# Kernel optimization log

Hardware: AMD Instinct MI355X
Metric: run time of the kernel (lower is better)

Reference implementation:

```python
import jax, jax.numpy as jnp
import numpy as np
from jax.scipy.linalg import expm

HIDDEN = 1024
STATE = 64
INTER = 4096
EPS = 1e-06
DT_MIN, DT_MAX = 0.001, 0.1


def rmsnorm(x, w, eps=EPS):
    var = jnp.mean(x * x, axis=-1, keepdims=True)
    return x * jax.lax.rsqrt(var + eps) * w


def setup_inputs() -> dict:
    key = jax.random.key(0)
    ks = jax.random.split(key, 10)
    hidden_states = jax.random.normal(ks[0], (4, 2048, HIDDEN), dtype=jnp.float32)
    A = jax.random.normal(ks[1], (STATE, STATE), dtype=jnp.float32) * 0.01
    B = jax.random.normal(ks[2], (STATE, HIDDEN), dtype=jnp.float32) * 0.01
    C = jax.random.normal(ks[3], (HIDDEN, STATE), dtype=jnp.float32) * 0.01
    D = jnp.ones((HIDDEN,), dtype=jnp.float32)
    log_dt = jax.random.uniform(ks[4], (HIDDEN,), dtype=jnp.float32) * (np.log(DT_MAX) - np.log(DT_MIN)) + np.log(DT_MIN)
    s = 1.0 / np.sqrt(HIDDEN)
    w_gate = jax.random.uniform(ks[5], (INTER, HIDDEN), minval=-s, maxval=s, dtype=jnp.float32)
    w_up = jax.random.uniform(ks[6], (INTER, HIDDEN), minval=-s, maxval=s, dtype=jnp.float32)
    s2 = 1.0 / np.sqrt(INTER)
    w_down = jax.random.uniform(ks[7], (HIDDEN, INTER), minval=-s2, maxval=s2, dtype=jnp.float32)
    ln1_w = jnp.ones((HIDDEN,), dtype=jnp.float32)
    ln2_w = jnp.ones((HIDDEN,), dtype=jnp.float32)
    return {"hidden_states": hidden_states, "A": A, "B": B, "C": C, "D": D,
            "log_dt": log_dt, "w_gate": w_gate, "w_up": w_up, "w_down": w_down,
            "ln1_w": ln1_w, "ln2_w": ln2_w}


def ssm(x, A, B, C, D, log_dt):
    # x: (batch, seq, hidden)
    dt = jnp.exp(log_dt)                    # (hidden,)
    A_bar = expm(A * jnp.mean(dt))          # (state, state)
    B_bar = B * dt[None, :]                 # (state, hidden)

    def step(state, x_t):
        # state: (batch, state); x_t: (batch, hidden)
        state = state @ A_bar.T + x_t @ B_bar.T
        out = state @ C.T + D * x_t
        return state, out

    x_t = jnp.swapaxes(x, 0, 1)             # (seq, batch, hidden)
    init = jnp.zeros((x.shape[0], A.shape[0]), dtype=x.dtype)
    _, ys = jax.lax.scan(step, init, x_t)
    return jnp.swapaxes(ys, 0, 1)           # (batch, seq, hidden)


def reference(hidden_states, A, B, C, D, log_dt, w_gate, w_up, w_down, ln1_w, ln2_w):
    # pre-norm SSM mixer + residual
    residual = hidden_states
    h = rmsnorm(hidden_states, ln1_w)
    h = ssm(h, A, B, C, D, log_dt)
    h = residual + h
    # pre-norm SwiGLU FFN + residual
    residual = h
    hn = rmsnorm(h, ln2_w)
    gate = hn @ w_gate.T
    up = hn @ w_up.T
    ffn = (jax.nn.silu(gate) * up) @ w_down.T
    return residual + ffn
```

## Files before the change

### kernel.cpp

```cpp
#include <hip/hip_runtime.h>
#include <hip/hip_bf16.h>
#include <math.h>

typedef __attribute__((ext_vector_type(8))) short short8;
typedef __attribute__((ext_vector_type(4))) float f32x4;
typedef __attribute__((ext_vector_type(4))) int int4v;
typedef __attribute__((ext_vector_type(8))) int int8v;

__device__ __forceinline__ unsigned short f2b(float x) {
  union { float f; unsigned int u; } v; v.f = x;
  unsigned int r = v.u + 0x7fffu + ((v.u >> 16) & 1u);
  return (unsigned short)(r >> 16);
}
__device__ __forceinline__ float b2f(unsigned short u) {
  union { unsigned int u; float f; } v; v.u = ((unsigned int)u) << 16;
  return v.f;
}
__device__ __forceinline__ unsigned char f2f8_sw(float x) {
  float a = fabsf(x);
  unsigned char s = (x < 0.f) ? 0x80 : 0x00;
  if (a >= 464.f) return s | 0x7E;
  union { float f; unsigned u; } v; v.f = a;
  int e = (int)(v.u >> 23) - 127;
  if (e < -6) {
    int q = (int)rintf(a * 512.f);
    if (q >= 8) return s | 0x08;
    return s | (unsigned char)q;
  }
  unsigned mant = v.u & 0x7FFFFF;
  unsigned keep = mant >> 20;
  unsigned rest = mant & 0xFFFFF;
  if (rest > 0x80000u || (rest == 0x80000u && (keep & 1))) keep++;
  unsigned exp8 = (unsigned)(e + 7);
  if (keep == 8) { keep = 0; exp8++; }
  if (exp8 >= 15 && keep >= 7) return s | 0x7E;
  return s | (unsigned char)((exp8 << 3) | keep);
}
#if __has_builtin(__builtin_amdgcn_cvt_pk_fp8_f32)
__device__ __forceinline__ unsigned char f2f8(float x) {
  return (unsigned char)(__builtin_amdgcn_cvt_pk_fp8_f32(x, x, 0, false) & 0xFF);
}
__device__ __forceinline__ unsigned int f8pack4(float a, float b, float c, float d) {
  int w0 = __builtin_amdgcn_cvt_pk_fp8_f32(a, b, 0, false);
  return (unsigned int)__builtin_amdgcn_cvt_pk_fp8_f32(c, d, w0, true);
}
#else
__device__ __forceinline__ unsigned char f2f8(float x) { return f2f8_sw(x); }
__device__ __forceinline__ unsigned int f8pack4(float a, float b, float c, float d) {
  return (unsigned)f2f8_sw(a) | ((unsigned)f2f8_sw(b) << 8) |
         ((unsigned)f2f8_sw(c) << 16) | ((unsigned)f2f8_sw(d) << 24);
}
#endif
__device__ __forceinline__ void async_ld16(const void* g, void* l) {
  __builtin_amdgcn_global_load_lds(
      (const __attribute__((address_space(1))) void*)g,
      (__attribute__((address_space(3))) void*)l, 16, 0, 0);
}

__device__ __forceinline__ f32x4 mx8(int8v a, int8v b, f32x4 c) {
#if __has_builtin(__builtin_amdgcn_mfma_scale_f32_16x16x128_f8f6f4)
  return __builtin_amdgcn_mfma_scale_f32_16x16x128_f8f6f4(
      a, b, c, 0, 0, 0, 0x7F7F7F7F, 0, 0x7F7F7F7F);
#else
  union { int8v v; long l[4]; } av, bv; av.v = a; bv.v = b;
#pragma unroll
  for (int j = 0; j < 4; j++)
    c = __builtin_amdgcn_mfma_f32_16x16x32_fp8_fp8(av.l[j], bv.l[j], c, 0, 0, 0);
  return c;
#endif
}

__device__ __forceinline__ int8v rd8(const unsigned char* tb, int r, int q) {
  union { int8v v; int4v h[2]; } x;
  x.h[0] = *(const int4v*)(tb + (size_t)((r << 3) + ((2 * q)     ^ (r & 7))) * 16);
  x.h[1] = *(const int4v*)(tb + (size_t)((r << 3) + ((2 * q + 1) ^ (r & 7))) * 16);
  return x.v;
}

__global__ __launch_bounds__(1024) void prep_combo(
    const float* __restrict__ A, const float* __restrict__ logdt,
    float* __restrict__ Abar, float* __restrict__ A64,
    const float* __restrict__ B, const float* __restrict__ Cm,
    unsigned short* __restrict__ Bb, unsigned short* __restrict__ Cb,
    const float* __restrict__ x, const float* __restrict__ w1,
    unsigned short* __restrict__ xnb, float* __restrict__ rs_out) {
  __shared__ float red[16];
  __shared__ float Ms[4096], T[4096], P[4096];
  __shared__ float wsum2[16];
  const int tid = threadIdx.x;
  if (blockIdx.x >= 33) {
    const int sub = tid >> 8, t = tid & 255;
    const size_t row = (size_t)(blockIdx.x - 33) * 4 + sub;
    const float4 v = ((const float4*)(x + row * 1024))[t];
    float ss = v.x * v.x + v.y * v.y + v.z * v.z + v.w * v.w;
#pragma unroll
    for (int off = 32; off > 0; off >>= 1) ss += __shfl_down(ss, off);
    if ((t & 63) == 0) wsum2[(sub << 2) | (t >> 6)] = ss;
    __syncthreads();
    const float tot = wsum2[sub << 2] + wsum2[(sub << 2) | 1] +
                      wsum2[(sub << 2) | 2] + wsum2[(sub << 2) | 3];
    const float rs = rsqrtf(tot * (1.f / 1024.f) + 1e-6f);
    if (t == 0) rs_out[row] = rs;
    const float4 wv = ((const float4*)w1)[t];
    ushort4 o;
    o.x = f2b(v.x * rs * wv.x); o.y = f2b(v.y * rs * wv.y);
    o.z = f2b(v.z * rs * wv.z); o.w = f2b(v.w * rs * wv.w);
    ((ushort4*)(xnb + row * 1024))[t] = o;
    return;
  }
  if (blockIdx.x != 0) {
    const size_t NB = 65536, NC = 65536;
    size_t base = (size_t)(blockIdx.x - 1) * 1024 + tid;
    const size_t stride = 32 * 1024;
    for (size_t id = base; id < NB + NC; id += stride) {
      if (id < NB) { int k = (int)(id & 1023); Bb[id] = f2b(B[id] * expf(logdt[k])); }
      else Cb[id - NB] = f2b(Cm[id - NB]);
    }
    return;
  }
  const int c = tid & 63;
  const int w = tid >> 6;
  float e = expf(logdt[tid]);
#pragma unroll
  for (int off = 32; off > 0; off >>= 1) e += __shfl_down(e, off);
  if (c == 0) red[w] = e;
  __syncthreads();
  if (tid == 0) {
    float s = 0.f;
    for (int i = 0; i < 16; i++) s += red[i];
    red[0] = s * (1.f / 1024.f);
  }
  __syncthreads();
  const float mdt = red[0];
  {
    float m0 = A[tid] * mdt, m1 = A[tid + 1024] * mdt,
          m2 = A[tid + 2048] * mdt, m3 = A[tid + 3072] * mdt;
    Ms[tid] = m0; Ms[tid + 1024] = m1; Ms[tid + 2048] = m2; Ms[tid + 3072] = m3;
    T[tid] = m0; T[tid + 1024] = m1; T[tid + 2048] = m2; T[tid + 3072] = m3;
    P[tid] = m0 + ((tid >> 6) == (tid & 63) ? 1.f : 0.f);
    P[tid + 1024] = m1 + (((tid + 1024) >> 6) == ((tid + 1024) & 63) ? 1.f : 0.f);
    P[tid + 2048] = m2 + (((tid + 2048) >> 6) == ((tid + 2048) & 63) ? 1.f : 0.f);
    P[tid + 3072] = m3 + (((tid + 3072) >> 6) == ((tid + 3072) & 63) ? 1.f : 0.f);
  }
  __syncthreads();
  float colM[64];
#pragma unroll
  for (int j = 0; j < 64; j++) colM[j] = Ms[j * 64 + c];
  for (int k = 2; k <= 6; k++) {
    const float inv = 1.f / (float)k;
    float accs[4];
#pragma unroll
    for (int i = 0; i < 4; i++) {
      const int r = w + 16 * i;
      const float4* Trow = (const float4*)(T + r * 64);
      float a0 = 0.f, a1 = 0.f, a2 = 0.f, a3 = 0.f;
#pragma unroll
      for (int j4 = 0; j4 < 16; j4++) {
        const float4 t = Trow[j4];
        a0 += t.x * colM[4 * j4 + 0]; a1 += t.y * colM[4 * j4 + 1];
        a2 += t.z * colM[4 * j4 + 2]; a3 += t.w * colM[4 * j4 + 3];
      }
      accs[i] = ((a0 + a1) + (a2 + a3)) * inv;
    }
    __syncthreads();
#pragma unroll
    for (int i = 0; i < 4; i++) {
      const int r = w + 16 * i;
      T[r * 64 + c] = accs[i];
      P[r * 64 + c] += accs[i];
    }
    __syncthreads();
  }
#pragma unroll
  for (int i = 0; i < 4; i++) {
    const int r = w + 16 * i;
    Abar[r * 64 + c] = P[r * 64 + c];
    T[r * 64 + c] = P[r * 64 + c];
  }
  __syncthreads();
  for (int sq = 0; sq < 6; sq++) {
    float colT[64];
#pragma unroll
    for (int j = 0; j < 64; j++) colT[j] = T[j * 64 + c];
    float accs[4];
#pragma unroll
    for (int i = 0; i < 4; i++) {
      const int r = w + 16 * i;
      const float4* Trow = (const float4*)(T + r * 64);
      float a0 = 0.f, a1 = 0.f, a2 = 0.f, a3 = 0.f;
#pragma unroll
      for (int j4 = 0; j4 < 16; j4++) {
        const float4 t = Trow[j4];
        a0 += t.x * colT[4 * j4 + 0]; a1 += t.y * colT[4 * j4 + 1];
        a2 += t.z * colT[4 * j4 + 2]; a3 += t.w * colT[4 * j4 + 3];
      }
      accs[i] = (a0 + a1) + (a2 + a3);
    }
    __syncthreads();
#pragma unroll
    for (int i = 0; i < 4; i++) T[(w + 16 * i) * 64 + c] = accs[i];
    __syncthreads();
  }
#pragma unroll
  for (int i = 0; i < 4; i++) {
    const int r = w + 16 * i;
    A64[r * 64 + c] = T[r * 64 + c];
  }
}

__global__ __launch_bounds__(256) void rmsnorm_f8(
    const float* __restrict__ x, const float* __restrict__ w,
    unsigned int* __restrict__ out) {
  const size_t row = blockIdx.x;
  const int tid = threadIdx.x;
  const float4 v = ((const float4*)(x + row * 1024))[tid];
  float ss = v.x * v.x + v.y * v.y + v.z * v.z + v.w * v.w;
#pragma unroll
  for (int off = 32; off > 0; off >>= 1) ss += __shfl_down(ss, off);
  __shared__ float wsum[4];
  if ((tid & 63) == 0) wsum[tid >> 6] = ss;
  __syncthreads();
  const float tot = wsum[0] + wsum[1] + wsum[2] + wsum[3];
  const float rs = rsqrtf(tot * (1.f / 1024.f) + 1e-6f);
  const float4 wv = ((const float4*)w)[tid];
  out[row * 256 + tid] =
      f8pack4(v.x * rs * wv.x, v.y * rs * wv.y, v.z * rs * wv.z, v.w * rs * wv.w);
}

template <int STORE_S>
__global__ __launch_bounds__(256) void scan_combo(
    const float* __restrict__ U, const float* __restrict__ Abar,
    const float* __restrict__ carry, float* __restrict__ zend,
    unsigned short* __restrict__ S,
    const float* __restrict__ csrc, unsigned char* __restrict__ cdst, size_t ccount) {
  constexpr int SCAN_BLOCKS = 32;
  __shared__ float s[4][64];
  if (blockIdx.x >= SCAN_BLOCKS) {
    size_t base = (size_t)(blockIdx.x - SCAN_BLOCKS) * 256 + threadIdx.x;
    size_t stride = (size_t)(gridDim.x - SCAN_BLOCKS) * 256;
    for (size_t id = base; id < ccount; id += stride)
      cdst[id] = f2f8(csrc[id] * 64.f);
    return;
  }
  const int wave = threadIdx.x >> 6, i = threadIdx.x & 63;
  const int task = blockIdx.x * 4 + wave;
  const int b = task >> 5, c = task & 31;
  float a[64];
#pragma unroll
  for (int j = 0; j < 64; j++) a[j] = Abar[i * 64 + j];
  float cur = STORE_S ? carry[(b * 32 + c) * 64 + i] : 0.f;
  const float* Ub = U + ((size_t)(b * 2048 + c * 64)) * 64;
  float u = Ub[i];
  for (int t = 0; t < 64; t++) {
    s[wave][i] = cur;
    float u_next = 0.f;
    if (t + 1 < 64) u_next = Ub[(t + 1) * 64 + i];
    const float4* s4 = (const float4*)s[wave];
    float a0 = u, a1 = 0.f, a2 = 0.f, a3 = 0.f;
#pragma unroll
    for (int j = 0; j < 16; j++) {
      float4 v = s4[j];
      a0 += a[4 * j + 0] * v.x; a1 += a[4 * j + 1] * v.y;
      a2 += a[4 * j + 2] * v.z; a3 += a[4 * j + 3] * v.w;
    }
    cur = (a0 + a1) + (a2 + a3);
    if (STORE_S) S[((size_t)(b * 2048 + c * 64 + t)) * 64 + i] = f2b(cur);
    u = u_next;
  }
  if (!STORE_S) zend[(b * 32 + c) * 64 + i] = cur;
}

__global__ __launch_bounds__(256) void carry_combo(
    const float* __restrict__ zend, const float* __restrict__ A64,
    float* __restrict__ carry,
    const float* __restrict__ csrc, unsigned char* __restrict__ cdst, size_t ccount) {
  __shared__ float s[4][64];
  if (blockIdx.x != 0) {
    size_t base = (size_t)(blockIdx.x - 1) * 256 + threadIdx.x;
    size_t stride = (size_t)(gridDim.x - 1) * 256;
    for (size_t id = base; id < ccount; id += stride)
      cdst[id] = f2f8(csrc[id] * 64.f);
    return;
  }
  const int b = threadIdx.x >> 6, i = threadIdx.x & 63;
  float a[64];
#pragma unroll
  for (int j = 0; j < 64; j++) a[j] = A64[i * 64 + j];
  float cur = 0.f;
  float z = zend[(b * 32 + 0) * 64 + i];
  for (int c = 0; c < 32; c++) {
    carry[(b * 32 + c) * 64 + i] = cur;
    s[b][i] = cur;
    float z_next = 0.f;
    if (c + 1 < 32) z_next = zend[(b * 32 + c + 1) * 64 + i];
    const float4* s4 = (const float4*)s[b];
    float a0 = z, a1 = 0.f, a2 = 0.f, a3 = 0.f;
#pragma unroll
    for (int j = 0; j < 16; j++) {
      float4 v = s4[j];
      a0 += a[4 * j + 0] * v.x; a1 += a[4 * j + 1] * v.y;
      a2 += a[4 * j + 2] * v.z; a3 += a[4 * j + 3] * v.w;
    }
    cur = (a0 + a1) + (a2 + a3);
    z = z_next;
  }
}

template <int BM, int BN, int WAVES_M, int WAVES_N, int EPI>
__global__ void __launch_bounds__(256) gemm_bt(
    const unsigned short* __restrict__ X, const unsigned short* __restrict__ W,
    int M, int N, int K,
    float* __restrict__ outf, const float* __restrict__ e_f,
    const float* __restrict__ e_d, const float* __restrict__ e_w,
    const float* __restrict__ e_r) {
  constexpr int BK = 64;
  constexpr int SM = BM / WAVES_M, SN = BN / WAVES_N;
  constexpr int TM = SM / 16, TN = SN / 16;
  __shared__ unsigned short aT[BM * BK];
  __shared__ unsigned short bT[BN * BK];
  const int tid = threadIdx.x;
  const int lane = tid & 63, wave = tid >> 6;
  const int wm = wave / WAVES_N, wn = wave % WAVES_N;
  const int lm = lane & 15, quad = lane >> 4;
  const long bm0 = (long)blockIdx.y * BM;
  const long bn0 = (long)blockIdx.x * BN;
  const int wb = tid & ~63;

  f32x4 acc[TM][TN];
#pragma unroll
  for (int i = 0; i < TM; i++)
#pragma unroll
    for (int j = 0; j < TN; j++) acc[i][j] = (f32x4){0.f, 0.f, 0.f, 0.f};

  for (int k0 = 0; k0 < K; k0 += BK) {
#pragma unroll
    for (int it = 0; it < (BM * 8) / 256; ++it) {
      int slot = it * 256 + tid;
      int r = slot >> 3, cp = slot & 7, c = cp ^ (r & 7);
      async_ld16(X + (bm0 + r) * (long)K + k0 + c * 8, aT + (it * 256 + wb) * 8);
    }
#pragma unroll
    for (int it = 0; it < (BN * 8) / 256; ++it) {
      int slot = it * 256 + tid;
      int r = slot >> 3, cp = slot & 7, c = cp ^ (r & 7);
      async_ld16(W + (bn0 + r) * (long)K + k0 + c * 8, bT + (it * 256 + wb) * 8);
    }
    __syncthreads();
#pragma unroll
    for (int kk = 0; kk < BK; kk += 32) {
      const int cch = (kk >> 3) + quad;
      short8 af[TM], bf[TN];
#pragma unroll
      for (int i = 0; i < TM; i++) {
        int r = wm * SM + i * 16 + lm;
        af[i] = *(const short8*)(aT + (r * 8 + (cch ^ (r & 7))) * 8);
      }
#pragma unroll
      for (int j = 0; j < TN; j++) {
        int r = wn * SN + j * 16 + lm;
        bf[j] = *(const short8*)(bT + (r * 8 + (cch ^ (r & 7))) * 8);
      }
#pragma unroll
      for (int i = 0; i < TM; i++)
#pragma unroll
        for (int j = 0; j < TN; j++)
          acc[i][j] = __builtin_amdgcn_mfma_f32_16x16x32_bf16(af[i], bf[j], acc[i][j], 0, 0, 0);
    }
    __syncthreads();
  }
#pragma unroll
  for (int i = 0; i < TM; i++) {
#pragma unroll
    for (int j = 0; j < TN; j++) {
#pragma unroll
      for (int r = 0; r < 4; r++) {
        const long m = bm0 + wm * SM + i * 16 + quad * 4 + r;
        const long n = bn0 + wn * SN + j * 16 + lm;
        const long idx = m * N + n;
        const float v = acc[i][j][r];
        if (EPI == 0) outf[idx] = v;
        else if (EPI == 5)
          outf[idx] = v + e_f[idx] * (1.f + e_d[n] * e_w[n] * e_r[m]);
      }
    }
  }
}

__global__ void __launch_bounds__(256) gemm_gu(
    const unsigned char* __restrict__ X, const unsigned char* __restrict__ Wg,
    const unsigned char* __restrict__ Wu, int M, int N, int K,
    unsigned char* __restrict__ out8, float inv) {
  constexpr int BM = 128, BN = 64, BK = 128;
  constexpr int TM = 4, TN = 2;
  __shared__ __attribute__((aligned(16))) unsigned char aT[BM * BK];
  __shared__ __attribute__((aligned(16))) unsigned char gT[BN * BK];
  __shared__ __attribute__((aligned(16))) unsigned char uT[BN * BK];
  const int tid = threadIdx.x;
  const int lane = tid & 63, wave = tid >> 6;
  const int wm = wave >> 1, wn = wave & 1;
  const int lm = lane & 15, quad = lane >> 4;
  const long bm0 = (long)blockIdx.y * BM;
  const long bn0 = (long)blockIdx.x * BN;
  const int wb = tid & ~63;

  f32x4 accg[TM][TN], accu[TM][TN];
#pragma unroll
  for (int i = 0; i < TM; i++)
#pragma unroll
    for (int j = 0; j < TN; j++) {
      accg[i][j] = (f32x4){0.f, 0.f, 0.f, 0.f};
      accu[i][j] = (f32x4){0.f, 0.f, 0.f, 0.f};
    }

  for (int k0 = 0; k0 < K; k0 += BK) {
#pragma unroll
    for (int it = 0; it < 4; ++it) {
      int slot = it * 256 + tid;
      int r = slot >> 3, cp = slot & 7, c = cp ^ (r & 7);
      async_ld16(X + (bm0 + r) * (long)K + k0 + c * 16, aT + (it * 256 + wb) * 16);
    }
#pragma unroll
    for (int it = 0; it < 2; ++it) {
      int slot = it * 256 + tid;
      int r = slot >> 3, cp = slot & 7, c = cp ^ (r & 7);
      async_ld16(Wg + (bn0 + r) * (long)K + k0 + c * 16, gT + (it * 256 + wb) * 16);
    }
#pragma unroll
    for (int it = 0; it < 2; ++it) {
      int slot = it * 256 + tid;
      int r = slot >> 3, cp = slot & 7, c = cp ^ (r & 7);
      async_ld16(Wu + (bn0 + r) * (long)K + k0 + c * 16, uT + (it * 256 + wb) * 16);
    }
    __syncthreads();
    int8v a[TM], g[TN], u[TN];
#pragma unroll
    for (int i = 0; i < TM; i++) a[i] = rd8(aT, wm * 64 + i * 16 + lm, quad);
#pragma unroll
    for (int j = 0; j < TN; j++) {
      g[j] = rd8(gT, wn * 32 + j * 16 + lm, quad);
      u[j] = rd8(uT, wn * 32 + j * 16 + lm, quad);
    }
#pragma unroll
    for (int i = 0; i < TM; i++)
#pragma unroll
      for (int j = 0; j < TN; j++) {
        accg[i][j] = mx8(a[i], g[j], accg[i][j]);
        accu[i][j] = mx8(a[i], u[j], accu[i][j]);
      }
    __syncthreads();
  }
#pragma unroll
  for (int i = 0; i < TM; i++) {
#pragma unroll
    for (int j = 0; j < TN; j++) {
#pragma unroll
      for (int r = 0; r < 4; r++) {
        const long m = bm0 + wm * 64 + i * 16 + quad * 4 + r;
        const long n = bn0 + wn * 32 + j * 16 + lm;
        const float gg = accg[i][j][r] * inv;
        const float uu = accu[i][j][r] * inv;
        const float s = gg / (1.f + __expf(-gg));
        out8[m * N + n] = f2f8(s * uu);
      }
    }
  }
}

__global__ void __launch_bounds__(256) gemm_f8(
    const unsigned char* __restrict__ X, const unsigned char* __restrict__ W,
    int M, int N, int K,
    float* __restrict__ outf, const float* __restrict__ e_f, float inv) {
  constexpr int BM = 128, BN = 64, BK = 128;
  constexpr int TM = 4, TN = 2;
  __shared__ __attribute__((aligned(16))) unsigned char aT[BM * BK];
  __shared__ __attribute__((aligned(16))) unsigned char bT[BN * BK];
  const int tid = threadIdx.x;
  const int lane = tid & 63, wave = tid >> 6;
  const int wm = wave >> 1, wn = wave & 1;
  const int lm = lane & 15, quad = lane >> 4;
  const long bm0 = (long)blockIdx.y * BM;
  const long bn0 = (long)blockIdx.x * BN;
  const int wb = tid & ~63;

  f32x4 acc[TM][TN];
#pragma unroll
  for (int i = 0; i < TM; i++)
#pragma unroll
    for (int j = 0; j < TN; j++) acc[i][j] = (f32x4){0.f, 0.f, 0.f, 0.f};

  for (int k0 = 0; k0 < K; k0 += BK) {
#pragma unroll
    for (int it = 0; it < 4; ++it) {
      int slot = it * 256 + tid;
      int r = slot >> 3, cp = slot & 7, c = cp ^ (r & 7);
      async_ld16(X + (bm0 + r) * (long)K + k0 + c * 16, aT + (it * 256 + wb) * 16);
    }
#pragma unroll
    for (int it = 0; it < 2; ++it) {
      int slot = it * 256 + tid;
      int r = slot >> 3, cp = slot & 7, c = cp ^ (r & 7);
      async_ld16(W + (bn0 + r) * (long)K + k0 + c * 16, bT + (it * 256 + wb) * 16);
    }
    __syncthreads();
    int8v a[TM], b[TN];
#pragma unroll
    for (int i = 0; i < TM; i++) a[i] = rd8(aT, wm * 64 + i * 16 + lm, quad);
#pragma unroll
    for (int j = 0; j < TN; j++) b[j] = rd8(bT, wn * 32 + j * 16 + lm, quad);
#pragma unroll
    for (int i = 0; i < TM; i++)
#pragma unroll
      for (int j = 0; j < TN; j++)
        acc[i][j] = mx8(a[i], b[j], acc[i][j]);
    __syncthreads();
  }
#pragma unroll
  for (int i = 0; i < TM; i++) {
#pragma unroll
    for (int j = 0; j < TN; j++) {
#pragma unroll
      for (int r = 0; r < 4; r++) {
        const long m = bm0 + wm * 64 + i * 16 + quad * 4 + r;
        const long n = bn0 + wn * 32 + j * 16 + lm;
        const long idx = m * N + n;
        outf[idx] = acc[i][j][r] * inv + e_f[idx];
      }
    }
  }
}

extern "C" void kernel_launch(void* const* d_in, const int* in_sizes, int n_in,
                              void* d_out, int out_size, void* d_ws, size_t ws_size,
                              hipStream_t stream) {
  const float* x     = (const float*)d_in[0];
  const float* A     = (const float*)d_in[1];
  const float* B     = (const float*)d_in[2];
  const float* C     = (const float*)d_in[3];
  const float* D     = (const float*)d_in[4];
  const float* logdt = (const float*)d_in[5];
  const float* wg    = (const float*)d_in[6];
  const float* wu    = (const float*)d_in[7];
  const float* wd    = (const float*)d_in[8];
  const float* ln1   = (const float*)d_in[9];
  const float* ln2   = (const float*)d_in[10];
  float* out = (float*)d_out;

  char* p = (char*)d_ws;
  auto alloc = [&](size_t bytes) { char* q = p; p += (bytes + 255) & ~(size_t)255; return q; };
  float* Abar  = (float*)alloc(64 * 64 * 4);
  float* A64   = (float*)alloc(64 * 64 * 4);
  float* zend  = (float*)alloc(4 * 32 * 64 * 4);
  float* carry = (float*)alloc(4 * 32 * 64 * 4);
  float* rs    = (float*)alloc((size_t)8192 * 4);
  float* U     = (float*)alloc((size_t)8192 * 64 * 4);
  unsigned short* S    = (unsigned short*)alloc((size_t)8192 * 64 * 2);
  unsigned short* Bb   = (unsigned short*)alloc((size_t)64 * 1024 * 2);
  unsigned short* Cb   = (unsigned short*)alloc((size_t)1024 * 64 * 2);
  unsigned char*  wg8  = (unsigned char*)alloc((size_t)4096 * 1024);
  unsigned char*  wu8  = (unsigned char*)alloc((size_t)4096 * 1024);
  unsigned char*  wd8  = (unsigned char*)alloc((size_t)1024 * 4096);
  unsigned short* xnb  = (unsigned short*)alloc((size_t)8192 * 1024 * 2);
  unsigned char*  hn8  = (unsigned char*)alloc((size_t)8192 * 1024);
  float* h             = (float*)alloc((size_t)8192 * 1024 * 4);
  unsigned char*  act8 = (unsigned char*)alloc((size_t)8192 * 4096);

  const size_t NWG = (size_t)4096 * 1024;

  prep_combo<<<33 + 2048, 1024, 0, stream>>>(
      A, logdt, Abar, A64, B, C, Bb, Cb, x, ln1, xnb, rs);
  gemm_bt<32, 64, 2, 2, 0><<<dim3(1, 256), 256, 0, stream>>>(
      xnb, Bb, 8192, 64, 1024, U, nullptr, nullptr, nullptr, nullptr);
  scan_combo<0><<<32 + 1024, 256, 0, stream>>>(
      U, Abar, nullptr, zend, S, wg, wg8, NWG);
  carry_combo<<<1 + 1024, 256, 0, stream>>>(zend, A64, carry, wu, wu8, NWG);
  scan_combo<1><<<32 + 1024, 256, 0, stream>>>(
      U, Abar, carry, zend, S, wd, wd8, NWG);
  gemm_bt<128, 128, 2, 2, 5><<<dim3(8, 64), 256, 0, stream>>>(
      S, Cb, 8192, 1024, 64, h, x, D, ln1, rs);
  rmsnorm_f8<<<8192, 256, 0, stream>>>(h, ln2, (unsigned int*)hn8);
  gemm_gu<<<dim3(64, 64), 256, 0, stream>>>(
      hn8, wg8, wu8, 8192, 4096, 1024, act8, 1.f / 64.f);
  gemm_f8<<<dim3(16, 64), 256, 0, stream>>>(
      act8, wd8, 8192, 1024, 4096, out, h, 1.f / 64.f);
}
```

Before: 397.5 us.

## Merge U-GEMM, scans, carry and weight casts into one cooperative kernel

Replaces four separate launches (small U GEMM, two chunk scans, carry propagation) with a single cooperative kernel of 512 blocks that uses grid-wide syncs between phases. Idle blocks in each phase convert weight matrices to fp8, and the first phase now overlaps half the gate-weight cast with the U GEMM. The aim is to cut launch gaps and tail idle time between the serial scan stages. The cost is grid-sync overhead, residency constraints from cooperative launch, and one scan phase now running alongside less cast work per block.

Measured after the change: 598.5 us. +50.6%, slower.

```diff
diff --git a/kernel.cpp b/kernel.cpp
--- a/kernel.cpp
+++ b/kernel.cpp
@@ -1,6 +1,9 @@
 #include <hip/hip_runtime.h>
 #include <hip/hip_bf16.h>
+#include <hip/hip_cooperative_groups.h>
 #include <math.h>
+
+namespace cg = cooperative_groups;
 
 typedef __attribute__((ext_vector_type(8))) short short8;
 typedef __attribute__((ext_vector_type(4))) float f32x4;
@@ -227,23 +230,105 @@
       f8pack4(v.x * rs * wv.x, v.y * rs * wv.y, v.z * rs * wv.z, v.w * rs * wv.w);
 }
 
+template <int BM, int BN, int WAVES_M, int WAVES_N, int EPI>
+__device__ __forceinline__ void gemm_bt_body(
+    const unsigned short* __restrict__ X, const unsigned short* __restrict__ W,
+    int M, int N, int K,
+    float* __restrict__ outf, const float* __restrict__ e_f,
+    const float* __restrict__ e_d, const float* __restrict__ e_w,
+    const float* __restrict__ e_r,
+    unsigned short* aT, unsigned short* bT, int bx, int by) {
+  constexpr int BK = 64;
+  constexpr int SM = BM / WAVES_M, SN = BN / WAVES_N;
+  constexpr int TM = SM / 16, TN = SN / 16;
+  const int tid = threadIdx.x;
+  const int lane = tid & 63, wave = tid >> 6;
+  const int wm = wave / WAVES_N, wn = wave % WAVES_N;
+  const int lm = lane & 15, quad = lane >> 4;
+  const long bm0 = (long)by * BM;
+  const long bn0 = (long)bx * BN;
+  const int wb = tid & ~63;
+
+  f32x4 acc[TM][TN];
+#pragma unroll
+  for (int i = 0; i < TM; i++)
+#pragma unroll
+    for (int j = 0; j < TN; j++) acc[i][j] = (f32x4){0.f, 0.f, 0.f, 0.f};
+
+  for (int k0 = 0; k0 < K; k0 += BK) {
+#pragma unroll
+    for (int it = 0; it < (BM * 8) / 256; ++it) {
+      int slot = it * 256 + tid;
+      int r = slot >> 3, cp = slot & 7, c = cp ^ (r & 7);
+      async_ld16(X + (bm0 + r) * (long)K + k0 + c * 8, aT + (it * 256 + wb) * 8);
+    }
+#pragma unroll
+    for (int it = 0; it < (BN * 8) / 256; ++it) {
+      int slot = it * 256 + tid;
+      int r = slot >> 3, cp = slot & 7, c = cp ^ (r & 7);
+      async_ld16(W + (bn0 + r) * (long)K + k0 + c * 8, bT + (it * 256 + wb) * 8);
+    }
+    __syncthreads();
+#pragma unroll
+    for (int kk = 0; kk < BK; kk += 32) {
+      const int cch = (kk >> 3) + quad;
+      short8 af[TM], bf[TN];
+#pragma unroll
+      for (int i = 0; i < TM; i++) {
+        int r = wm * SM + i * 16 + lm;
+        af[i] = *(const short8*)(aT + (r * 8 + (cch ^ (r & 7))) * 8);
+      }
+#pragma unroll
+      for (int j = 0; j < TN; j++) {
+        int r = wn * SN + j * 16 + lm;
+        bf[j] = *(const short8*)(bT + (r * 8 + (cch ^ (r & 7))) * 8);
+      }
+#pragma unroll
+      for (int i = 0; i < TM; i++)
+#pragma unroll
+        for (int j = 0; j < TN; j++)
+          acc[i][j] = __builtin_amdgcn_mfma_f32_16x16x32_bf16(af[i], bf[j], acc[i][j], 0, 0, 0);
+    }
+    __syncthreads();
+  }
+#pragma unroll
+  for (int i = 0; i < TM; i++) {
+#pragma unroll
+    for (int j = 0; j < TN; j++) {
+#pragma unroll
+      for (int r = 0; r < 4; r++) {
+        const long m = bm0 + wm * SM + i * 16 + quad * 4 + r;
+        const long n = bn0 + wn * SN + j * 16 + lm;
+        const long idx = m * N + n;
+        const float v = acc[i][j][r];
+        if (EPI == 0) outf[idx] = v;
+        else if (EPI == 5)
+          outf[idx] = v + e_f[idx] * (1.f + e_d[n] * e_w[n] * e_r[m]);
+      }
+    }
+  }
+}
+
+template <int BM, int BN, int WAVES_M, int WAVES_N, int EPI>
+__global__ void __launch_bounds__(256) gemm_bt(
+    const unsigned short* __restrict__ X, const unsigned short* __restrict__ W,
+    int M, int N, int K,
+    float* __restrict__ outf, const float* __restrict__ e_f,
+    const float* __restrict__ e_d, const float* __restrict__ e_w,
+    const float* __restrict__ e_r) {
+  __shared__ unsigned short aT[BM * 64];
+  __shared__ unsigned short bT[BN * 64];
+  gemm_bt_body<BM, BN, WAVES_M, WAVES_N, EPI>(
+      X, W, M, N, K, outf, e_f, e_d, e_w, e_r, aT, bT, blockIdx.x, blockIdx.y);
+}
+
 template <int STORE_S>
-__global__ __launch_bounds__(256) void scan_combo(
+__device__ __forceinline__ void scan_body(
     const float* __restrict__ U, const float* __restrict__ Abar,
     const float* __restrict__ carry, float* __restrict__ zend,
-    unsigned short* __restrict__ S,
-    const float* __restrict__ csrc, unsigned char* __restrict__ cdst, size_t ccount) {
-  constexpr int SCAN_BLOCKS = 32;
-  __shared__ float s[4][64];
-  if (blockIdx.x >= SCAN_BLOCKS) {
-    size_t base = (size_t)(blockIdx.x - SCAN_BLOCKS) * 256 + threadIdx.x;
-    size_t stride = (size_t)(gridDim.x - SCAN_BLOCKS) * 256;
-    for (size_t id = base; id < ccount; id += stride)
-      cdst[id] = f2f8(csrc[id] * 64.f);
-    return;
-  }
+    unsigned short* __restrict__ S, float (*s)[64], int blk) {
   const int wave = threadIdx.x >> 6, i = threadIdx.x & 63;
-  const int task = blockIdx.x * 4 + wave;
+  const int task = blk * 4 + wave;
   const int b = task >> 5, c = task & 31;
   float a[64];
 #pragma unroll
@@ -270,18 +355,9 @@
   if (!STORE_S) zend[(b * 32 + c) * 64 + i] = cur;
 }
 
-__global__ __launch_bounds__(256) void carry_combo(
+__device__ __forceinline__ void carry_body(
     const float* __restrict__ zend, const float* __restrict__ A64,
-    float* __restrict__ carry,
-    const float* __restrict__ csrc, unsigned char* __restrict__ cdst, size_t ccount) {
-  __shared__ float s[4][64];
-  if (blockIdx.x != 0) {
-    size_t base = (size_t)(blockIdx.x - 1) * 256 + threadIdx.x;
-    size_t stride = (size_t)(gridDim.x - 1) * 256;
-    for (size_t id = base; id < ccount; id += stride)
-      cdst[id] = f2f8(csrc[id] * 64.f);
-    return;
-  }
+    float* __restrict__ carry, float (*s)[64]) {
   const int b = threadIdx.x >> 6, i = threadIdx.x & 63;
   float a[64];
 #pragma unroll
@@ -306,83 +382,54 @@
   }
 }
 
-template <int BM, int BN, int WAVES_M, int WAVES_N, int EPI>
-__global__ void __launch_bounds__(256) gemm_bt(
-    const unsigned short* __restrict__ X, const unsigned short* __restrict__ W,
-    int M, int N, int K,
-    float* __restrict__ outf, const float* __restrict__ e_f,
-    const float* __restrict__ e_d, const float* __restrict__ e_w,
-    const float* __restrict__ e_r) {
-  constexpr int BK = 64;
-  constexpr int SM = BM / WAVES_M, SN = BN / WAVES_N;
-  constexpr int TM = SM / 16, TN = SN / 16;
-  __shared__ unsigned short aT[BM * BK];
-  __shared__ unsigned short bT[BN * BK];
+__global__ void __launch_bounds__(256, 2) mid_coop(
+    const unsigned short* __restrict__ xnb, const unsigned short* __restrict__ Bb,
+    float* __restrict__ U,
+    const float* __restrict__ Abar, const float* __restrict__ A64,
+    float* __restrict__ zend, float* __restrict__ carry,
+    unsigned short* __restrict__ S,
+    const float* __restrict__ wg, unsigned char* __restrict__ wg8,
+    const float* __restrict__ wu, unsigned char* __restrict__ wu8,
+    const float* __restrict__ wd, unsigned char* __restrict__ wd8) {
+  __shared__ __attribute__((aligned(16))) unsigned char smem[12288];
+  unsigned short* aT = (unsigned short*)smem;
+  unsigned short* bT = (unsigned short*)(smem + 4096);
+  float (*sscan)[64] = (float(*)[64])smem;
+  const size_t NWG = (size_t)4096 * 1024;
+  const int bid = blockIdx.x;
   const int tid = threadIdx.x;
-  const int lane = tid & 63, wave = tid >> 6;
-  const int wm = wave / WAVES_N, wn = wave % WAVES_N;
-  const int lm = lane & 15, quad = lane >> 4;
-  const long bm0 = (long)blockIdx.y * BM;
-  const long bn0 = (long)blockIdx.x * BN;
-  const int wb = tid & ~63;
-
-  f32x4 acc[TM][TN];
-#pragma unroll
-  for (int i = 0; i < TM; i++)
-#pragma unroll
-    for (int j = 0; j < TN; j++) acc[i][j] = (f32x4){0.f, 0.f, 0.f, 0.f};
-
-  for (int k0 = 0; k0 < K; k0 += BK) {
-#pragma unroll
-    for (int it = 0; it < (BM * 8) / 256; ++it) {
-      int slot = it * 256 + tid;
-      int r = slot >> 3, cp = slot & 7, c = cp ^ (r & 7);
-      async_ld16(X + (bm0 + r) * (long)K + k0 + c * 8, aT + (it * 256 + wb) * 8);
-    }
-#pragma unroll
-    for (int it = 0; it < (BN * 8) / 256; ++it) {
-      int slot = it * 256 + tid;
-      int r = slot >> 3, cp = slot & 7, c = cp ^ (r & 7);
-      async_ld16(W + (bn0 + r) * (long)K + k0 + c * 8, bT + (it * 256 + wb) * 8);
-    }
-    __syncthreads();
-#pragma unroll
-    for (int kk = 0; kk < BK; kk += 32) {
-      const int cch = (kk >> 3) + quad;
-      short8 af[TM], bf[TN];
-#pragma unroll
-      for (int i = 0; i < TM; i++) {
-        int r = wm * SM + i * 16 + lm;
-        af[i] = *(const short8*)(aT + (r * 8 + (cch ^ (r & 7))) * 8);
-      }
-#pragma unroll
-      for (int j = 0; j < TN; j++) {
-        int r = wn * SN + j * 16 + lm;
-        bf[j] = *(const short8*)(bT + (r * 8 + (cch ^ (r & 7))) * 8);
-      }
-#pragma unroll
-      for (int i = 0; i < TM; i++)
-#pragma unroll
-        for (int j = 0; j < TN; j++)
-          acc[i][j] = __builtin_amdgcn_mfma_f32_16x16x32_bf16(af[i], bf[j], acc[i][j], 0, 0, 0);
-    }
-    __syncthreads();
-  }
-#pragma unroll
-  for (int i = 0; i < TM; i++) {
-#pragma unroll
-    for (int j = 0; j < TN; j++) {
-#pragma unroll
-      for (int r = 0; r < 4; r++) {
-        const long m = bm0 + wm * SM + i * 16 + quad * 4 + r;
-        const long n = bn0 + wn * SN + j * 16 + lm;
-        const long idx = m * N + n;
-        const float v = acc[i][j][r];
-        if (EPI == 0) outf[idx] = v;
-        else if (EPI == 5)
-          outf[idx] = v + e_f[idx] * (1.f + e_d[n] * e_w[n] * e_r[m]);
-      }
-    }
+
+  if (bid < 256) {
+    gemm_bt_body<32, 64, 2, 2, 0>(xnb, Bb, 8192, 64, 1024, U,
+                                  nullptr, nullptr, nullptr, nullptr, aT, bT, 0, bid);
+  } else {
+    size_t base = (size_t)(bid - 256) * 256 + tid;
+    for (size_t id = base; id < NWG / 2; id += (size_t)256 * 256)
+      wg8[id] = f2f8(wg[id] * 64.f);
+  }
+  cg::this_grid().sync();
+  if (bid < 32) {
+    scan_body<0>(U, Abar, nullptr, zend, S, sscan, bid);
+  } else {
+    size_t base = NWG / 2 + (size_t)(bid - 32) * 256 + tid;
+    for (size_t id = base; id < NWG; id += (size_t)480 * 256)
+      wg8[id] = f2f8(wg[id] * 64.f);
+  }
+  cg::this_grid().sync();
+  if (bid == 0) {
+    carry_body(zend, A64, carry, sscan);
+  } else {
+    size_t base = (size_t)(bid - 1) * 256 + tid;
+    for (size_t id = base; id < NWG; id += (size_t)511 * 256)
+      wu8[id] = f2f8(wu[id] * 64.f);
+  }
+  cg::this_grid().sync();
+  if (bid < 32) {
+    scan_body<1>(U, Abar, carry, zend, S, sscan, bid);
+  } else {
+    size_t base = (size_t)(bid - 32) * 256 + tid;
+    for (size_t id = base; id < NWG; id += (size_t)480 * 256)
+      wd8[id] = f2f8(wd[id] * 64.f);
   }
 }
 
@@ -564,17 +611,16 @@
   float* h             = (float*)alloc((size_t)8192 * 1024 * 4);
   unsigned char*  act8 = (unsigned char*)alloc((size_t)8192 * 4096);
 
-  const size_t NWG = (size_t)4096 * 1024;
-
   prep_combo<<<33 + 2048, 1024, 0, stream>>>(
       A, logdt, Abar, A64, B, C, Bb, Cb, x, ln1, xnb, rs);
-  gemm_bt<32, 64, 2, 2, 0><<<dim3(1, 256), 256, 0, stream>>>(
-      xnb, Bb, 8192, 64, 1024, U, nullptr, nullptr, nullptr, nullptr);
-  scan_combo<0><<<32 + 1024, 256, 0, stream>>>(
-      U, Abar, nullptr, zend, S, wg, wg8, NWG);
-  carry_combo<<<1 + 1024, 256, 0, stream>>>(zend, A64, carry, wu, wu8, NWG);
-  scan_combo<1><<<32 + 1024, 256, 0, stream>>>(
-      U, Abar, carry, zend, S, wd, wd8, NWG);
+  {
+    void* cargs[] = {(void*)&xnb, (void*)&Bb, (void*)&U, (void*)&Abar, (void*)&A64,
+                     (void*)&zend, (void*)&carry, (void*)&S,
+                     (void*)&wg, (void*)&wg8, (void*)&wu, (void*)&wu8,
+                     (void*)&wd, (void*)&wd8};
+    hipLaunchCooperativeKernel((const void*)mid_coop, dim3(512), dim3(256),
+                               cargs, 0, stream);
+  }
   gemm_bt<128, 128, 2, 2, 5><<<dim3(8, 64), 256, 0, stream>>>(
       S, Cb, 8192, 1024, 64, h, x, D, ln1, rs);
   rmsnorm_f8<<<8192, 256, 0, stream>>>(h, ln2, (unsigned int*)hn8);
```
